# Kernel optimization log

Hardware: AMD Instinct MI355X
Metric: run time of the kernel (lower is better)

Reference implementation:

```python
import jax, jax.numpy as jnp
import numpy as np

NUM_DENSE = 13
NUM_SPARSE = 26
FEAT_NUM = 40000  # categories per sparse field
FEATURE_LENGTH = NUM_SPARSE * FEAT_NUM + NUM_DENSE  # 1_040_013
K = 64
BATCH = 4096


def setup_inputs() -> dict:
    key = jax.random.key(0)
    k1, k2, k3, k4 = jax.random.split(key, 4)
    dense_inputs = jax.random.normal(k1, (BATCH, NUM_DENSE), dtype=jnp.float32)
    sparse_inputs = jax.random.randint(k2, (BATCH, NUM_SPARSE), 0, FEAT_NUM, dtype=jnp.int64)
    w0 = jnp.zeros((1,), dtype=jnp.float32)
    w = jax.random.normal(k3, (FEATURE_LENGTH, 1), dtype=jnp.float32) * 0.05
    V = jax.random.normal(k4, (K, FEATURE_LENGTH), dtype=jnp.float32) * 0.05
    return {"dense_inputs": dense_inputs, "sparse_inputs": sparse_inputs, "w0": w0, "w": w, "V": V}


def reference(dense_inputs, sparse_inputs, w0, w, V):
    # Feature layout matches the original concat order: [dense (NUM_DENSE) | one-hot field 0 | ... | one-hot field 25].
    # The one-hot @ matrix products are computed as row gathers (mathematically identical,
    # since one_hot(i) @ M == M[i]).
    offsets = NUM_DENSE + FEAT_NUM * jnp.arange(NUM_SPARSE, dtype=sparse_inputs.dtype)
    idx = sparse_inputs + offsets[None, :]  # [B, NUM_SPARSE] global row ids into feature_length

    # ---- first order: w0 + stack @ w ----
    w_dense = w[:NUM_DENSE]            # [ND, 1]
    first = w0 + dense_inputs @ w_dense + jnp.sum(w[idx, 0], axis=1, keepdims=True)  # [B,1]

    # ---- second order: 0.5 * sum((stack @ V^T)^2 - (stack^2 @ (V^T)^2), axis=1) ----
    Vt = V.T                           # [F, K]
    Vt_dense = Vt[:NUM_DENSE]          # [ND, K]
    Vt_sparse = Vt[idx]                # [B, NUM_SPARSE, K] gathered latent vectors

    sv = dense_inputs @ Vt_dense + jnp.sum(Vt_sparse, axis=1)                 # [B, K]
    # stack^2 for the one-hot block equals the one-hot block itself (0/1 entries)
    s2v2 = (dense_inputs ** 2) @ (Vt_dense ** 2) + jnp.sum(Vt_sparse ** 2, axis=1)  # [B, K]

    second = 0.5 * jnp.sum(sv ** 2 - s2v2, axis=1, keepdims=True)  # [B,1]
    return first + second
```

## Files before the change

### kernel.cpp

```cpp
#include <hip/hip_runtime.h>

#define NUM_DENSE 13
#define NUM_SPARSE 26
#define FEAT_NUM 40000
#define FEATURE_LENGTH (NUM_SPARSE * FEAT_NUM + NUM_DENSE)
#define KDIM 64
#define BATCH 4096
#define QSIZE 4000
#define NCHUNK 10
#define LDSN (QSIZE + 4)
#define NT 1024
#define NG 8
#define NBUF 4

__global__ void transpose_kernel(const int* __restrict__ sp, int* __restrict__ sp_t) {
    int tid = blockIdx.x * blockDim.x + threadIdx.x;
    int j = tid >> 12;
    int b = tid & 4095;
    sp_t[tid] = sp[b * NUM_SPARSE + j];
}

__device__ __forceinline__ void load_lds16(const float4* g, float* l) {
    __builtin_amdgcn_global_load_lds(
        (const __attribute__((address_space(1))) void*)g,
        (__attribute__((address_space(3))) void*)l, 16, 0, 0);
}

__global__ __launch_bounds__(NT, 8) void accum_kernel(const float* __restrict__ V,
                                                      const int* __restrict__ sp_t,
                                                      float* __restrict__ PS,
                                                      float* __restrict__ PQ) {
    __shared__ __align__(16) float buf[NBUF][LDSN];

    const int k = blockIdx.x;
    const int g = blockIdx.y;
    const int tid = threadIdx.x;
    const int jstart = (g * NUM_SPARSE) / NG;
    const int jend   = ((g + 1) * NUM_SPARSE) / NG;
    const int nw     = jend - jstart;

    const size_t kbase = (size_t)k * FEATURE_LENGTH + NUM_DENSE;
    const int a   = (int)(kbase & 3);
    const int nl4 = (QSIZE + a + 3) >> 2;
    const int nstage = nw * NCHUNK;

    int s0[4], s1[4], s2[4], s3[4];
#pragma unroll
    for (int r = 0; r < 4; ++r) {
        s0[r] = sp_t[(jstart + 0) * BATCH + tid + NT * r];
        s1[r] = sp_t[(jstart + 1) * BATCH + tid + NT * r];
        s2[r] = sp_t[(jstart + 2) * BATCH + tid + NT * r];
    }
    if (nw == 4) {
#pragma unroll
        for (int r = 0; r < 4; ++r) s3[r] = sp_t[(jstart + 3) * BATCH + tid + NT * r];
    } else {
#pragma unroll
        for (int r = 0; r < 4; ++r) s3[r] = 0;
    }

    float sAcc[4] = {0.f, 0.f, 0.f, 0.f};
    float qAcc[4] = {0.f, 0.f, 0.f, 0.f};
    int cs[4];
#pragma unroll
    for (int r = 0; r < 4; ++r) cs[r] = s0[r];

    __syncthreads();

    auto issue = [&](int t) {
        const int w = t / NCHUNK;
        const int q = t - w * NCHUNK;
        const float4* __restrict__ g4 =
            (const float4*)(V + (kbase + (size_t)(jstart + w) * FEAT_NUM
                                       + (size_t)q * QSIZE) - a);
        if (tid < nl4)
            load_lds16(g4 + tid, &buf[t & 3][4 * tid]);
    };

    issue(0);
    issue(1);

    int wg = 0, qg = 0;
    for (int s = 0; s < nstage; ++s) {
        const int t = s + 2;
        if (t < nstage) issue(t);

        const int ahead = nstage - 1 - s;
        if (ahead >= 2)      asm volatile("s_waitcnt vmcnt(2)" ::: "memory");
        else if (ahead == 1) asm volatile("s_waitcnt vmcnt(1)" ::: "memory");
        else                 asm volatile("s_waitcnt vmcnt(0)" ::: "memory");
        __builtin_amdgcn_s_barrier();
        asm volatile("" ::: "memory");

        const int q0 = qg * QSIZE;
        const float* __restrict__ bb = buf[s & 3];
#pragma unroll
        for (int r = 0; r < 4; ++r) {
            int rel = cs[r] - q0;
            bool in = (rel >= 0) && (rel < QSIZE);
            int addr = in ? (rel + a) : 0;
            float v = bb[addr];
            v = in ? v : 0.f;
            sAcc[r] += v;
            qAcc[r] += v * v;
        }

        if (++qg == NCHUNK) {
            qg = 0; ++wg;
            if (wg < nw) {
#pragma unroll
                for (int r = 0; r < 4; ++r)
                    cs[r] = (wg == 1) ? s1[r] : (wg == 2) ? s2[r] : s3[r];
            }
        }
    }

    const int base = (g * KDIM + k) * BATCH + tid;
#pragma unroll
    for (int r = 0; r < 4; ++r) {
        PS[base + NT * r] = sAcc[r];
        PQ[base + NT * r] = qAcc[r];
    }
}

__global__ __launch_bounds__(256) void final_kernel(const float* __restrict__ dense,
                                                    const float* __restrict__ w0,
                                                    const float* __restrict__ w,
                                                    const float* __restrict__ V,
                                                    const int* __restrict__ sp_t,
                                                    const float* __restrict__ PS,
                                                    const float* __restrict__ PQ,
                                                    float* __restrict__ out) {
    __shared__ float red[16][17];
    const int tid = threadIdx.x;
    const int bi  = tid & 15;
    const int ki  = tid >> 4;
    const int b   = blockIdx.x * 16 + bi;

    float x[NUM_DENSE], x2[NUM_DENSE];
#pragma unroll
    for (int d = 0; d < NUM_DENSE; ++d) {
        x[d]  = dense[b * NUM_DENSE + d];
        x2[d] = x[d] * x[d];
    }

    float t = 0.f;
#pragma unroll
    for (int kk = 0; kk < 4; ++kk) {
        const int k = ki * 4 + kk;
        float sv = 0.f, qv = 0.f;
#pragma unroll
        for (int g = 0; g < NG; ++g) {
            sv += PS[((g << 6) + k) * BATCH + b];
            qv += PQ[((g << 6) + k) * BATCH + b];
        }
        const float* __restrict__ Vk = V + (size_t)k * FEATURE_LENGTH;
#pragma unroll
        for (int d = 0; d < NUM_DENSE; ++d) {
            float vv = Vk[d];
            sv += x[d] * vv;
            qv += x2[d] * vv * vv;
        }
        t += sv * sv - qv;
    }
    red[bi][ki] = 0.5f * t;
    __syncthreads();

    if (tid < 16) {
        const int bb = blockIdx.x * 16 + tid;
        float acc = w0[0];
#pragma unroll
        for (int i = 0; i < 16; ++i) acc += red[tid][i];
#pragma unroll
        for (int j = 0; j < NUM_SPARSE; ++j)
            acc += w[NUM_DENSE + j * FEAT_NUM + sp_t[j * BATCH + bb]];
#pragma unroll
        for (int d = 0; d < NUM_DENSE; ++d) acc += x[d] * w[d];
        out[bb] = acc;
    }
}

extern "C" void kernel_launch(void* const* d_in, const int* in_sizes, int n_in,
                              void* d_out, int out_size, void* d_ws, size_t ws_size,
                              hipStream_t stream) {
    const float* dense  = (const float*)d_in[0];
    const int*   sparse = (const int*)d_in[1];
    const float* w0     = (const float*)d_in[2];
    const float* w      = (const float*)d_in[3];
    const float* V      = (const float*)d_in[4];
    float* out = (float*)d_out;

    char* ws = (char*)d_ws;
    int*   sp_t = (int*)ws;
    float* PS   = (float*)(ws + (1 << 20));
    float* PQ   = (float*)(ws + (1 << 20) + NG * KDIM * BATCH * 4);

    transpose_kernel<<<(NUM_SPARSE * BATCH) / 256, 256, 0, stream>>>(sparse, sp_t);
    accum_kernel<<<dim3(KDIM, NG), NT, 0, stream>>>(V, sp_t, PS, PQ);
    final_kernel<<<BATCH / 16, 256, 0, stream>>>(dense, w0, w, V, sp_t, PS, PQ, out);
}
```

Measured before the change: 393.2 us.

## Stage V chunks through registers with deeper lookahead instead of direct-to-LDS loads

Replaces the global_load_lds direct-to-LDS async copies with explicit global_load_dwordx4 into a ring of four registers, keeping four chunks in flight. Each chunk is written to LDS one stage ahead of when it is consumed. The goal is more memory-level parallelism and less load latency exposed per stage while streaming V. In exchange it costs extra VGPRs and LDS write instructions, and it relies on hand-written waitcnt bookkeeping, which could break correctness if the counts are wrong.

```diff
diff --git a/kernel.cpp b/kernel.cpp
--- a/kernel.cpp
+++ b/kernel.cpp
@@ -12,6 +12,7 @@
 #define NT 1024
 #define NG 8
 #define NBUF 4
+#define LA 4
 
 __global__ void transpose_kernel(const int* __restrict__ sp, int* __restrict__ sp_t) {
     int tid = blockIdx.x * blockDim.x + threadIdx.x;
@@ -20,10 +21,16 @@
     sp_t[tid] = sp[b * NUM_SPARSE + j];
 }
 
-__device__ __forceinline__ void load_lds16(const float4* g, float* l) {
-    __builtin_amdgcn_global_load_lds(
-        (const __attribute__((address_space(1))) void*)g,
-        (__attribute__((address_space(3))) void*)l, 16, 0, 0);
+__device__ __forceinline__ float4 gload16(const float4* p) {
+    float4 r;
+    asm volatile("global_load_dwordx4 %0, %1, off"
+                 : "=&v"(r)
+                 : "v"((const __attribute__((address_space(1))) float4*)p));
+    return r;
+}
+
+__device__ __forceinline__ void swrite16(float* lp, float4 v) {
+    *reinterpret_cast<float4*>(lp) = v;
 }
 
 __global__ __launch_bounds__(NT, 8) void accum_kernel(const float* __restrict__ V,
@@ -44,6 +51,9 @@
     const int nl4 = (QSIZE + a + 3) >> 2;
     const int nstage = nw * NCHUNK;
 
+    const float4* g4b = (const float4*)(V + kbase + (size_t)jstart * FEAT_NUM - a) + tid;
+    const bool ld = (tid < nl4);
+
     int s0[4], s1[4], s2[4], s3[4];
 #pragma unroll
     for (int r = 0; r < 4; ++r) {
@@ -67,50 +77,56 @@
 
     __syncthreads();
 
-    auto issue = [&](int t) {
-        const int w = t / NCHUNK;
-        const int q = t - w * NCHUNK;
-        const float4* __restrict__ g4 =
-            (const float4*)(V + (kbase + (size_t)(jstart + w) * FEAT_NUM
-                                       + (size_t)q * QSIZE) - a);
-        if (tid < nl4)
-            load_lds16(g4 + tid, &buf[t & 3][4 * tid]);
-    };
-
-    issue(0);
-    issue(1);
+    float4 R[4];
+    if (ld) {
+        R[0] = gload16(g4b);
+        R[1] = gload16(g4b + 1000);
+        R[2] = gload16(g4b + 2000);
+        R[3] = gload16(g4b + 3000);
+    }
+    asm volatile("s_waitcnt vmcnt(3)" ::: "memory");
+    if (ld) swrite16(&buf[0][4 * tid], R[0]);
 
     int wg = 0, qg = 0;
-    for (int s = 0; s < nstage; ++s) {
-        const int t = s + 2;
-        if (t < nstage) issue(t);
-
-        const int ahead = nstage - 1 - s;
-        if (ahead >= 2)      asm volatile("s_waitcnt vmcnt(2)" ::: "memory");
-        else if (ahead == 1) asm volatile("s_waitcnt vmcnt(1)" ::: "memory");
-        else                 asm volatile("s_waitcnt vmcnt(0)" ::: "memory");
-        __builtin_amdgcn_s_barrier();
-        asm volatile("" ::: "memory");
-
-        const int q0 = qg * QSIZE;
-        const float* __restrict__ bb = buf[s & 3];
-#pragma unroll
-        for (int r = 0; r < 4; ++r) {
-            int rel = cs[r] - q0;
-            bool in = (rel >= 0) && (rel < QSIZE);
-            int addr = in ? (rel + a) : 0;
-            float v = bb[addr];
-            v = in ? v : 0.f;
-            sAcc[r] += v;
-            qAcc[r] += v * v;
-        }
-
-        if (++qg == NCHUNK) {
-            qg = 0; ++wg;
-            if (wg < nw) {
-#pragma unroll
-                for (int r = 0; r < 4; ++r)
-                    cs[r] = (wg == 1) ? s1[r] : (wg == 2) ? s2[r] : s3[r];
+    for (int sb = 0; sb < nstage; sb += 4) {
+#pragma unroll
+        for (int u = 0; u < 4; ++u) {
+            const int s = sb + u;
+            if (s < nstage) {
+                if (s + LA < nstage && ld)
+                    R[u] = gload16(g4b + (size_t)(s + LA) * 1000);
+                if (s + 1 < nstage) {
+                    const int pend = (nstage - 2 - s < 3) ? (nstage - 2 - s) : 3;
+                    if (pend == 3)      asm volatile("s_waitcnt vmcnt(3)" ::: "memory");
+                    else if (pend == 2) asm volatile("s_waitcnt vmcnt(2)" ::: "memory");
+                    else if (pend == 1) asm volatile("s_waitcnt vmcnt(1)" ::: "memory");
+                    else                asm volatile("s_waitcnt vmcnt(0)" ::: "memory");
+                    if (ld) swrite16(&buf[(u + 1) & 3][4 * tid], R[(u + 1) & 3]);
+                }
+                asm volatile("s_waitcnt lgkmcnt(0)" ::: "memory");
+                __builtin_amdgcn_s_barrier();
+                asm volatile("" ::: "memory");
+
+                const int q0 = qg * QSIZE;
+                const float* __restrict__ bb = buf[u];
+#pragma unroll
+                for (int r = 0; r < 4; ++r) {
+                    int rel = cs[r] - q0;
+                    bool in = (rel >= 0) && (rel < QSIZE);
+                    int addr = in ? (rel + a) : 0;
+                    float v = bb[addr];
+                    v = in ? v : 0.f;
+                    sAcc[r] += v;
+                    qAcc[r] += v * v;
+                }
+                if (++qg == NCHUNK) {
+                    qg = 0; ++wg;
+                    if (wg < nw) {
+#pragma unroll
+                        for (int r = 0; r < 4; ++r)
+                            cs[r] = (wg == 1) ? s1[r] : (wg == 2) ? s2[r] : s3[r];
+                    }
+                }
             }
         }
     }
```

After: 389.4 us. No clear change (-1.0%).
